# Kernel tuning notes

Measured on AMD Instinct MI355X. Metric: run time of the kernel, lower is better.

## Reference

```python
import jax, jax.numpy as jnp
import numpy as np

N_HID = 256
N_IN = 2
N_OUT = 2
BATCH = 256
LENGTH = 1024
ALPHA = 0.25
SIGMA_NEU = 0.05
N_CON = 6553


def setup_inputs() -> dict:
    key = jax.random.key(0)
    k1, k2, k3, k4, k5 = jax.random.split(key, 5)
    rng = np.random.RandomState(0)
    # masked recurrent weight pieces (match torch __init__ construction)
    w_0 = rng.randn(N_HID, N_HID) / np.sqrt(N_HID)
    abs_w_0 = jnp.asarray(np.abs(w_0), dtype=jnp.float32)
    is_con_np = np.zeros((N_HID, N_HID), dtype=np.float32)
    ind_in = rng.choice(np.arange(N_HID), size=N_CON)
    ind_out = rng.choice(np.arange(N_HID), size=N_CON)
    is_con_np[ind_in, ind_out] = 1.0
    w_sign = jnp.asarray(np.sign(rng.randn(N_HID, N_HID)), dtype=jnp.float32)
    is_con = jnp.asarray(is_con_np)
    return {
        "input_signal": jax.random.normal(k1, (BATCH, LENGTH, N_IN), dtype=jnp.float32),
        "hidden": jnp.zeros((BATCH, N_HID), dtype=jnp.float32),
        "w_in": jax.random.normal(k2, (N_HID, N_IN), dtype=jnp.float32) / np.sqrt(N_IN),
        "w_out": jax.random.normal(k3, (N_OUT, N_HID), dtype=jnp.float32) / np.sqrt(N_HID),
        "abs_w_0": abs_w_0,
        "w_sign": w_sign,
        "is_con": is_con,
    }


def reference(input_signal, hidden, w_in, w_out, abs_w_0, w_sign, is_con):
    # masked signed recurrent weight: theta = |w0| * mask; w_hh = sign * theta where mask>0
    theta = abs_w_0 * is_con
    w_hh = jnp.where(is_con > 0, w_sign * theta, jnp.zeros_like(theta))  # [H,H]

    alpha = jnp.full((N_HID,), ALPHA, dtype=input_signal.dtype)
    x = jnp.transpose(input_signal, (1, 0, 2))  # [T,B,I]
    # input projection for all timesteps at once (w_in has no bias)
    inp_proj = jnp.einsum("tbi,hi->tbh", x, w_in)  # [T,B,H]
    # iid per-step neural noise: randn * sigma * sqrt(alpha)
    noise = (jax.random.normal(jax.random.key(42), (LENGTH, BATCH, N_HID), dtype=input_signal.dtype)
             * SIGMA_NEU * jnp.sqrt(alpha))

    def step(h, uv):
        u, n = uv
        tmp = u + jnp.tanh(h) @ w_hh.T  # F.linear(tanh(h), w_hh)
        h_new = (1.0 - alpha) * h + alpha * tmp + n
        return h_new, h_new

    h_last, hs = jax.lax.scan(step, hidden, (inp_proj, noise))  # hs: [T,B,H]
    outputs = jnp.einsum("tbh,oh->tbo", hs, w_out)  # [T,B,O]
    hidden_list = jnp.transpose(hs, (1, 0, 2))  # [B,T,H]
    output_list = jnp.transpose(outputs, (1, 0, 2))  # [B,T,O]
    return hidden_list, output_list, h_last
```

## Files before the change

kernel.cpp:

```cpp
#include <hip/hip_runtime.h>
#include <stdint.h>

#define TT 1024
#define HB 256
#define NE 48
#define NE2 24
#define O1 67108864u
#define O2 (67108864u + 524288u)

__device__ __forceinline__ uint32_t rotl32(uint32_t x, uint32_t r){ return (x<<r)|(x>>(32u-r)); }

#define RND(r) { x0+=x1; x1=rotl32(x1,(r)); x1^=x0; }
__device__ __forceinline__ void tf_h1g(uint32_t k0,uint32_t k1,uint32_t ks2,uint32_t& x0,uint32_t& x1){
  x0 += k0; x1 += k1;
  RND(13) RND(15) RND(26) RND(6)  x0+=k1;  x1+=ks2+1u;
  RND(17) RND(29) RND(16) RND(24) x0+=ks2; x1+=k0+2u;
  RND(13) RND(15) RND(26) RND(6)  x0+=k0;  x1+=k1+3u;
}
__device__ __forceinline__ void tf_h2g(uint32_t k0,uint32_t k1,uint32_t ks2,uint32_t& x0,uint32_t& x1){
  RND(17) RND(29) RND(16) RND(24) x0+=k1;  x1+=ks2+4u;
  RND(13) RND(15) RND(26) RND(6)  x0+=ks2; x1+=k0+5u;
}
__device__ __forceinline__ void tf2x32(uint32_t k0,uint32_t k1,uint32_t& x0,uint32_t& x1){
  const uint32_t ks2 = 0x1BD11BDAu ^ k0 ^ k1;
  tf_h1g(k0,k1,ks2,x0,x1); tf_h2g(k0,k1,ks2,x0,x1);
}
__device__ __forceinline__ void tf_h1(uint32_t& x0, uint32_t& x1){ tf_h1g(0u,42u,0x1BD11BF0u,x0,x1); }
__device__ __forceinline__ void tf_h2(uint32_t& x0, uint32_t& x1){ tf_h2g(0u,42u,0x1BD11BF0u,x0,x1); }
#undef RND

__device__ __forceinline__ float bits_to_noise(uint32_t bits){
  float f = __uint_as_float((bits>>9) | 0x3F800000u) - 1.0f;
  const float lo = -0.99999994f;
  float x = fmaxf(fmaf(f, 1.99999994f, lo), lo);
  float m = (1.0f - x) * (1.0f + x);
  float w = -0.69314718056f * __log2f(m);
  float p;
  if (w < 5.0f){
    w -= 2.5f;
    p = 2.81022636e-08f;
    p = fmaf(p, w, 3.43273939e-07f);
    p = fmaf(p, w, -3.5233877e-06f);
    p = fmaf(p, w, -4.39150654e-06f);
    p = fmaf(p, w, 0.00021858087f);
    p = fmaf(p, w, -0.00125372503f);
    p = fmaf(p, w, -0.00417768164f);
    p = fmaf(p, w, 0.246640727f);
    p = fmaf(p, w, 1.50140941f);
  } else {
    w = __fsqrt_rn(w) - 3.0f;
    p = -0.000200214257f;
    p = fmaf(p, w, 0.000100950558f);
    p = fmaf(p, w, 0.00134934322f);
    p = fmaf(p, w, -0.00367342844f);
    p = fmaf(p, w, 0.00573950773f);
    p = fmaf(p, w, -0.0076224613f);
    p = fmaf(p, w, 0.00943887047f);
    p = fmaf(p, w, 1.00167406f);
    p = fmaf(p, w, 2.83297682f);
  }
  return 0.035355339059f * (p * x);
}

__global__ void init_flags(uint32_t* flags){
  if (flags) { flags[0]=0u; flags[1]=0u; }
}

__global__ void check_kernel(float* out, const uint32_t* flags){
  uint32_t a0=0u, a1=0u;                 tf2x32(0u,0u,a0,a1);
  uint32_t b0=0xffffffffu, b1=0xffffffffu; tf2x32(0xffffffffu,0xffffffffu,b0,b1);
  uint32_t c0=0x243f6a88u, c1=0x85a308d3u; tf2x32(0x13198a2eu,0x03707344u,c0,c1);
  if (!(a0==0x6b200159u && a1==0x99ba4efeu)) out[0] = 1e30f;
  if (!(b0==0x1cb996fcu && b1==0xbb002be7u)) out[1] = 2e30f;
  if (!(c0==0xc4923a9cu && c1==0x483df7a0u)) out[2] = 3e30f;
  uint32_t d0=7u, d1=9u; tf_h1(d0,d1); tf_h2(d0,d1);
  uint32_t e0=7u, e1=9u; tf2x32(0u,42u,e0,e1);
  if (!(d0==e0 && d1==e1)) out[3] = 4e30f;
  if (flags && flags[0]) out[5] = 6e30f;
}

__launch_bounds__(1024)
__global__ void rnn_kernel(const float* __restrict__ input_signal,
                           const float* __restrict__ hidden0,
                           const float* __restrict__ w_in,
                           const float* __restrict__ w_out,
                           const float* __restrict__ abs_w0,
                           const float* __restrict__ w_sign,
                           const float* __restrict__ is_con,
                           float* __restrict__ out,
                           uint32_t* __restrict__ flags)
{
  __shared__ float    ew[HB][NE];
  __shared__ uint16_t ei[HB][NE];
  __shared__ float    xbuf[TT*2];
  __shared__ float    hstage[16][HB];
  __shared__ float    nbuf[4][HB];
  __shared__ float    tbuf[2][HB];
  __shared__ int      cnts[HB];
  __shared__ int      rankinv[HB];
  __shared__ int      rof4[HB];
  __shared__ float    wot0[HB], wot1[HB];

  const int tid = threadIdx.x;
  const int b   = blockIdx.x;
  const bool gw = (tid < 512);

  {
    const float* xg = input_signal + (uint64_t)b*TT*2;
    *(float2*)(xbuf + tid*2) = *(const float2*)(xg + tid*2);
  }
  if (tid < HB){
    int c = 0;
    const float* ic = is_con + tid*HB;
    for (int k = 0; k < HB; k += 4){
      float4 c4 = *(const float4*)(ic + k);
      c += (c4.x>0.f)+(c4.y>0.f)+(c4.z>0.f)+(c4.w>0.f);
    }
    cnts[tid] = c;
    if (c > NE && flags) flags[0] = 1u;
  }
  __syncthreads();

  if (tid < HB){
    int myc = cnts[tid], r = 0;
    for (int k = 0; k < HB; ++k){
      int ck = cnts[k];
      r += (int)((ck > myc) || (ck == myc && k < tid));
    }
    rankinv[r] = tid;
    rof4[tid]  = r << 2;
  }
  __syncthreads();

  uint32_t bj = 0u, ax0 = 0u, ax1 = 0u;
  if (tid < HB){
    const int j = tid;
    const float* ic = is_con + j*HB;
    const float* aw = abs_w0 + j*HB;
    const float* ws = w_sign + j*HB;
    int n = 0;
    for (int k = 0; k < HB; ++k){
      if (ic[k] > 0.f && n < NE){
        ew[j][n] = ws[k]*aw[k];
        ei[j][n] = (uint16_t)rof4[k];
        ++n;
      }
    }
    for (int s = n; s < NE; ++s){ ew[j][s] = 0.f; ei[j][s] = (uint16_t)rof4[j]; }
    wot0[rof4[j]>>2] = w_out[j];
    wot1[rof4[j]>>2] = w_out[HB + j];
  } else if (tid >= 512){
    int m2 = tid - 512, rn = m2 >> 1, qn = m2 & 1;
    bj = (uint32_t)b*256u + (uint32_t)rankinv[rn];
    if (qn == 0){
      uint32_t x0 = 0u, x1 = bj;
      tf2x32(0u, 42u, x0, x1);
      nbuf[0][rn] = bits_to_noise(x0 ^ x1);
    } else {
      ax0 = 0u; ax1 = 65536u + bj;
      tf_h1(ax0, ax1);
    }
  }
  __syncthreads();

  float    pwv[NE2];
  uint32_t piv[NE2/2];
  int trip = 0, row = 0, q = 0, rr = 0;
  float h = 0.f, wi0 = 0.f, wi1 = 0.f;
  float4 wo0 = {0,0,0,0}, wo1 = {0,0,0,0};
  int rf0 = 0, rf1 = 0;
  {
    int j0 = (tid & 127) << 1;
    rf0 = rof4[j0]; rf1 = rof4[j0+1];
  }
  if (gw){
    rr = tid >> 1; q = tid & 1;
    row = rankinv[rr];
    int c = cnts[row]; if (c > NE) c = NE;
    uint16_t pad = (uint16_t)rof4[row];
    uint32_t cur = 0u;
    #pragma unroll
    for (int s = 0; s < NE2; ++s){
      int idx = 2*s + q;
      float w = 0.f; uint32_t o = pad;
      if (idx < c){ w = ew[row][idx]; o = ei[row][idx]; }
      pwv[s] = w;
      if (s & 1) piv[s>>1] = cur | (o << 16); else cur = o;
    }
    trip = __builtin_amdgcn_readfirstlane((c + 1) >> 1);
    if (q == 0){
      h   = hidden0[b*HB + row];
      wi0 = w_in[row*2]; wi1 = w_in[row*2 + 1];
      tbuf[0][rr] = 1.0f - 2.0f/(__expf(2.0f*h) + 1.0f);
    }
  } else {
    int m2 = tid - 512;
    if (m2 < 128){
      int lam = m2 & 63;
      wo0 = *(const float4*)(wot0 + lam*4);
      wo1 = *(const float4*)(wot1 + lam*4);
    }
  }
  float* hrow = out + (uint64_t)b*TT*HB;
  float* orow = out + O1 + (uint64_t)b*TT*2;
  __syncthreads();

  for (int t = 0; t < TT; ++t){
    const int par = t & 1;
    if (gw){
      __builtin_amdgcn_s_setprio(1);
      const char* tb = (const char*)(&tbuf[par][0]);
      float tv[NE2];
      #pragma unroll
      for (int s = 0; s < NE2; s += 2){
        if (s < trip){
          uint32_t pa = piv[s>>1];
          tv[s]   = *(const float*)(tb + (pa & 0xFFFFu));
          tv[s+1] = *(const float*)(tb + (pa >> 16));
        }
      }
      float y0 = 0.f, y1 = 0.f;
      #pragma unroll
      for (int s = 0; s < NE2; s += 2){
        if (s < trip){
          y0 = fmaf(pwv[s],   tv[s],   y0);
          y1 = fmaf(pwv[s+1], tv[s+1], y1);
        }
      }
      float y = y0 + y1;
      y += __shfl_xor(y, 1, 64);
      if (q == 0){
        float nz = nbuf[t&3][rr];
        float2 xv = *(const float2*)(xbuf + t*2);
        float u  = fmaf(xv.x, wi0, xv.y*wi1);
        h = fmaf(0.25f, u + y, 0.75f*h) + nz;
        hstage[t&15][rr] = h;
        tbuf[par^1][rr] = 1.0f - 2.0f/(__expf(2.0f*h) + 1.0f);
      }
      __builtin_amdgcn_s_setprio(0);
    } else {
      int m2 = tid - 512, rn = m2 >> 1, qn = m2 & 1;
      if (((t+1) & 1) == qn){
        if (t + 1 < TT){
          uint32_t f0 = ax0, f1 = ax1;
          tf_h2(f0, f1);
          nbuf[(t+1)&3][rn] = bits_to_noise(f0 ^ f1);
        }
      } else {
        if (t + 2 < TT){
          ax0 = 0u; ax1 = (uint32_t)(t+2)*65536u + bj;
          tf_h1(ax0, ax1);
        }
      }
      if (m2 < 128 && (t & 1)){
        int tau = t - 2 + (m2 >> 6);
        if (tau >= 0){
          int lam = m2 & 63;
          float4 hv = *(const float4*)(&hstage[tau&15][lam*4]);
          float p0 = hv.x*wo0.x + hv.y*wo0.y + hv.z*wo0.z + hv.w*wo0.w;
          float p1 = hv.x*wo1.x + hv.y*wo1.y + hv.z*wo1.z + hv.w*wo1.w;
          #pragma unroll
          for (int d = 1; d < 64; d <<= 1){
            p0 += __shfl_xor(p0, d, 64);
            p1 += __shfl_xor(p1, d, 64);
          }
          if (lam == 0) *(float2*)(orow + tau*2) = make_float2(p0, p1);
        }
      }
    }
    __syncthreads();

    if ((t & 7) == 7 && t >= 15){
      int s  = tid >> 7;
      int j0 = (tid & 127) << 1;
      int rbase = t - 15;
      const char* hs = (const char*)(&hstage[(rbase + s)&15][0]);
      float2 v;
      v.x = *(const float*)(hs + rf0);
      v.y = *(const float*)(hs + rf1);
      *(float2*)(hrow + (uint64_t)(rbase + s)*HB + j0) = v;
    }
  }

  {
    int s  = tid >> 7;
    int j0 = (tid & 127) << 1;
    const char* hs = (const char*)(&hstage[(1016 + s)&15][0]);
    float2 v;
    v.x = *(const float*)(hs + rf0);
    v.y = *(const float*)(hs + rf1);
    *(float2*)(hrow + (uint64_t)(1016 + s)*HB + j0) = v;
  }
  if (!gw){
    int m2 = tid - 512;
    if (m2 < 64){
      float4 hv = *(const float4*)(&hstage[1023&15][m2*4]);
      float p0 = hv.x*wo0.x + hv.y*wo0.y + hv.z*wo0.z + hv.w*wo0.w;
      float p1 = hv.x*wo1.x + hv.y*wo1.y + hv.z*wo1.z + hv.w*wo1.w;
      #pragma unroll
      for (int d = 1; d < 64; d <<= 1){
        p0 += __shfl_xor(p0, d, 64);
        p1 += __shfl_xor(p1, d, 64);
      }
      if (m2 == 0) *(float2*)(orow + (TT-1)*2) = make_float2(p0, p1);
    }
  }
  if (gw && q == 0) out[O2 + b*HB + row] = h;
}

extern "C" void kernel_launch(void* const* d_in, const int* in_sizes, int n_in,
                              void* d_out, int out_size, void* d_ws, size_t ws_size,
                              hipStream_t stream) {
  const float* input_signal = (const float*)d_in[0];
  const float* hidden       = (const float*)d_in[1];
  const float* w_in         = (const float*)d_in[2];
  const float* w_out        = (const float*)d_in[3];
  const float* abs_w0       = (const float*)d_in[4];
  const float* w_sign       = (const float*)d_in[5];
  const float* is_con       = (const float*)d_in[6];
  float* out = (float*)d_out;
  uint32_t* flags = (ws_size >= 8) ? (uint32_t*)d_ws : nullptr;

  init_flags<<<1, 1, 0, stream>>>(flags);
  rnn_kernel<<<256, 1024, 0, stream>>>(input_signal, hidden, w_in, w_out,
                                       abs_w0, w_sign, is_con, out, flags);
  check_kernel<<<1, 1, 0, stream>>>(out, flags);
}
```

Measured before the change: 929.1 us.

## Restructure noise generation, gather addressing, and output staging in RNN loop

Noise threads now compute the full Threefry hash for two future steps on even iterations instead of splitting it into halves across iterations, and run the output projection on odd iterations. Output projections are staged in shared memory and written to global memory in batches every 8 steps along with the hidden states. Gather offsets are kept as full 32-bit per-edge registers with the buffer parity split into two specialised branches, and the setprio hints are removed. The changes aim to cut per-step ALU and global-store work on the critical path, at the cost of more registers and a shifted flush schedule.

```diff
diff --git a/kernel.cpp b/kernel.cpp
--- a/kernel.cpp
+++ b/kernel.cpp
@@ -11,22 +11,15 @@
 __device__ __forceinline__ uint32_t rotl32(uint32_t x, uint32_t r){ return (x<<r)|(x>>(32u-r)); }
 
 #define RND(r) { x0+=x1; x1=rotl32(x1,(r)); x1^=x0; }
-__device__ __forceinline__ void tf_h1g(uint32_t k0,uint32_t k1,uint32_t ks2,uint32_t& x0,uint32_t& x1){
+__device__ __forceinline__ void tf2x32(uint32_t k0,uint32_t k1,uint32_t& x0,uint32_t& x1){
+  const uint32_t ks2 = 0x1BD11BDAu ^ k0 ^ k1;
   x0 += k0; x1 += k1;
   RND(13) RND(15) RND(26) RND(6)  x0+=k1;  x1+=ks2+1u;
   RND(17) RND(29) RND(16) RND(24) x0+=ks2; x1+=k0+2u;
   RND(13) RND(15) RND(26) RND(6)  x0+=k0;  x1+=k1+3u;
-}
-__device__ __forceinline__ void tf_h2g(uint32_t k0,uint32_t k1,uint32_t ks2,uint32_t& x0,uint32_t& x1){
   RND(17) RND(29) RND(16) RND(24) x0+=k1;  x1+=ks2+4u;
   RND(13) RND(15) RND(26) RND(6)  x0+=ks2; x1+=k0+5u;
 }
-__device__ __forceinline__ void tf2x32(uint32_t k0,uint32_t k1,uint32_t& x0,uint32_t& x1){
-  const uint32_t ks2 = 0x1BD11BDAu ^ k0 ^ k1;
-  tf_h1g(k0,k1,ks2,x0,x1); tf_h2g(k0,k1,ks2,x0,x1);
-}
-__device__ __forceinline__ void tf_h1(uint32_t& x0, uint32_t& x1){ tf_h1g(0u,42u,0x1BD11BF0u,x0,x1); }
-__device__ __forceinline__ void tf_h2(uint32_t& x0, uint32_t& x1){ tf_h2g(0u,42u,0x1BD11BF0u,x0,x1); }
 #undef RND
 
 __device__ __forceinline__ float bits_to_noise(uint32_t bits){
@@ -73,9 +66,6 @@
   if (!(a0==0x6b200159u && a1==0x99ba4efeu)) out[0] = 1e30f;
   if (!(b0==0x1cb996fcu && b1==0xbb002be7u)) out[1] = 2e30f;
   if (!(c0==0xc4923a9cu && c1==0x483df7a0u)) out[2] = 3e30f;
-  uint32_t d0=7u, d1=9u; tf_h1(d0,d1); tf_h2(d0,d1);
-  uint32_t e0=7u, e1=9u; tf2x32(0u,42u,e0,e1);
-  if (!(d0==e0 && d1==e1)) out[3] = 4e30f;
   if (flags && flags[0]) out[5] = 6e30f;
 }
 
@@ -96,6 +86,7 @@
   __shared__ float    hstage[16][HB];
   __shared__ float    nbuf[4][HB];
   __shared__ float    tbuf[2][HB];
+  __shared__ float    obuf[16][2];
   __shared__ int      cnts[HB];
   __shared__ int      rankinv[HB];
   __shared__ int      rof4[HB];
@@ -132,7 +123,7 @@
   }
   __syncthreads();
 
-  uint32_t bj = 0u, ax0 = 0u, ax1 = 0u;
+  uint32_t bj = 0u;
   if (tid < HB){
     const int j = tid;
     const float* ic = is_con + j*HB;
@@ -156,36 +147,30 @@
       uint32_t x0 = 0u, x1 = bj;
       tf2x32(0u, 42u, x0, x1);
       nbuf[0][rn] = bits_to_noise(x0 ^ x1);
-    } else {
-      ax0 = 0u; ax1 = 65536u + bj;
-      tf_h1(ax0, ax1);
     }
   }
   __syncthreads();
 
   float    pwv[NE2];
-  uint32_t piv[NE2/2];
+  uint32_t adr[NE2];
   int trip = 0, row = 0, q = 0, rr = 0;
   float h = 0.f, wi0 = 0.f, wi1 = 0.f;
   float4 wo0 = {0,0,0,0}, wo1 = {0,0,0,0};
   int rf0 = 0, rf1 = 0;
-  {
-    int j0 = (tid & 127) << 1;
-    rf0 = rof4[j0]; rf1 = rof4[j0+1];
-  }
+  const int j0 = (tid & 127) << 1;
+  rf0 = rof4[j0]; rf1 = rof4[j0+1];
   if (gw){
     rr = tid >> 1; q = tid & 1;
     row = rankinv[rr];
     int c = cnts[row]; if (c > NE) c = NE;
-    uint16_t pad = (uint16_t)rof4[row];
-    uint32_t cur = 0u;
+    uint32_t pad = (uint32_t)rof4[row];
     #pragma unroll
     for (int s = 0; s < NE2; ++s){
       int idx = 2*s + q;
       float w = 0.f; uint32_t o = pad;
       if (idx < c){ w = ew[row][idx]; o = ei[row][idx]; }
       pwv[s] = w;
-      if (s & 1) piv[s>>1] = cur | (o << 16); else cur = o;
+      adr[s] = o;
     }
     trip = __builtin_amdgcn_readfirstlane((c + 1) >> 1);
     if (q == 0){
@@ -208,51 +193,44 @@
   for (int t = 0; t < TT; ++t){
     const int par = t & 1;
     if (gw){
-      __builtin_amdgcn_s_setprio(1);
-      const char* tb = (const char*)(&tbuf[par][0]);
-      float tv[NE2];
-      #pragma unroll
-      for (int s = 0; s < NE2; s += 2){
-        if (s < trip){
-          uint32_t pa = piv[s>>1];
-          tv[s]   = *(const float*)(tb + (pa & 0xFFFFu));
-          tv[s+1] = *(const float*)(tb + (pa >> 16));
+      float nz = nbuf[t&3][rr];
+      float2 xv = *(const float2*)(xbuf + t*2);
+      float y0 = 0.f, y1 = 0.f;
+      if (par == 0){
+        #pragma unroll
+        for (int s = 0; s < NE2; s += 2){
+          if (s < trip){
+            y0 = fmaf(pwv[s],   *(const float*)((const char*)tbuf + adr[s]),   y0);
+            y1 = fmaf(pwv[s+1], *(const float*)((const char*)tbuf + adr[s+1]), y1);
+          }
         }
-      }
-      float y0 = 0.f, y1 = 0.f;
-      #pragma unroll
-      for (int s = 0; s < NE2; s += 2){
-        if (s < trip){
-          y0 = fmaf(pwv[s],   tv[s],   y0);
-          y1 = fmaf(pwv[s+1], tv[s+1], y1);
+      } else {
+        #pragma unroll
+        for (int s = 0; s < NE2; s += 2){
+          if (s < trip){
+            y0 = fmaf(pwv[s],   *(const float*)((const char*)tbuf + 1024 + adr[s]),   y0);
+            y1 = fmaf(pwv[s+1], *(const float*)((const char*)tbuf + 1024 + adr[s+1]), y1);
+          }
         }
       }
       float y = y0 + y1;
       y += __shfl_xor(y, 1, 64);
       if (q == 0){
-        float nz = nbuf[t&3][rr];
-        float2 xv = *(const float2*)(xbuf + t*2);
-        float u  = fmaf(xv.x, wi0, xv.y*wi1);
+        float u = fmaf(xv.x, wi0, xv.y*wi1);
         h = fmaf(0.25f, u + y, 0.75f*h) + nz;
         hstage[t&15][rr] = h;
         tbuf[par^1][rr] = 1.0f - 2.0f/(__expf(2.0f*h) + 1.0f);
       }
-      __builtin_amdgcn_s_setprio(0);
     } else {
-      int m2 = tid - 512, rn = m2 >> 1, qn = m2 & 1;
-      if (((t+1) & 1) == qn){
-        if (t + 1 < TT){
-          uint32_t f0 = ax0, f1 = ax1;
-          tf_h2(f0, f1);
-          nbuf[(t+1)&3][rn] = bits_to_noise(f0 ^ f1);
+      int m2 = tid - 512;
+      if (!(t & 1)){
+        int tv = t + 1 + (m2 & 1);
+        if (tv < TT){
+          uint32_t x0 = 0u, x1 = (uint32_t)tv*65536u + bj;
+          tf2x32(0u, 42u, x0, x1);
+          nbuf[tv&3][m2>>1] = bits_to_noise(x0 ^ x1);
         }
-      } else {
-        if (t + 2 < TT){
-          ax0 = 0u; ax1 = (uint32_t)(t+2)*65536u + bj;
-          tf_h1(ax0, ax1);
-        }
-      }
-      if (m2 < 128 && (t & 1)){
+      } else if (m2 < 128){
         int tau = t - 2 + (m2 >> 6);
         if (tau >= 0){
           int lam = m2 & 63;
@@ -264,32 +242,43 @@
             p0 += __shfl_xor(p0, d, 64);
             p1 += __shfl_xor(p1, d, 64);
           }
-          if (lam == 0) *(float2*)(orow + tau*2) = make_float2(p0, p1);
+          if (lam == 0){ obuf[tau&15][0] = p0; obuf[tau&15][1] = p1; }
         }
       }
     }
     __syncthreads();
 
-    if ((t & 7) == 7 && t >= 15){
+    if ((t & 7) == 7){
       int s  = tid >> 7;
-      int j0 = (tid & 127) << 1;
-      int rbase = t - 15;
-      const char* hs = (const char*)(&hstage[(rbase + s)&15][0]);
+      int fr = t - 14 + s;
+      if (fr >= 0){
+        const char* hs = (const char*)(&hstage[fr&15][0]);
+        float2 v;
+        v.x = *(const float*)(hs + rf0);
+        v.y = *(const float*)(hs + rf1);
+        *(float2*)(hrow + (uint64_t)fr*HB + j0) = v;
+      }
+      if (tid < 16){
+        int so = tid >> 1, fo = t - 14 + so;
+        if (fo >= 0) orow[fo*2 + (tid&1)] = obuf[fo&15][tid&1];
+      }
+    }
+  }
+
+  {
+    int s  = tid >> 7;
+    if (s >= 1){
+      int fr = 1016 + s;
+      const char* hs = (const char*)(&hstage[fr&15][0]);
       float2 v;
       v.x = *(const float*)(hs + rf0);
       v.y = *(const float*)(hs + rf1);
-      *(float2*)(hrow + (uint64_t)(rbase + s)*HB + j0) = v;
-    }
-  }
-
-  {
-    int s  = tid >> 7;
-    int j0 = (tid & 127) << 1;
-    const char* hs = (const char*)(&hstage[(1016 + s)&15][0]);
-    float2 v;
-    v.x = *(const float*)(hs + rf0);
-    v.y = *(const float*)(hs + rf1);
-    *(float2*)(hrow + (uint64_t)(1016 + s)*HB + j0) = v;
+      *(float2*)(hrow + (uint64_t)fr*HB + j0) = v;
+    }
+  }
+  if (tid < 12){
+    int s = tid >> 1;
+    orow[(1017+s)*2 + (tid&1)] = obuf[(1017+s)&15][tid&1];
   }
   if (!gw){
     int m2 = tid - 512;
```

Result: no change. 929.1 us (+0.0%).
